# Kernel optimization log

Measured on AMD Instinct MI355X. Metric: run time of the kernel, lower is better.

## Reference

```python
import jax, jax.numpy as jnp
import numpy as np

EPS = 1e-5
GROUPS = 128  # 4 bands * nearest_power_of_2_divisor(256, 32)

def _haar_bands(x):
    # x: (C, H, W), H and W even -> SAME pad is a no-op for 2x2 stride-2 conv.
    # lax conv is cross-correlation: band[i,j] = sum_ab x[2i+a, 2j+b] * k[a,b]
    C, H, W = x.shape
    xr = x.reshape(C, H // 2, 2, W // 2, 2)
    x00 = xr[:, :, 0, :, 0]; x01 = xr[:, :, 0, :, 1]
    x10 = xr[:, :, 1, :, 0]; x11 = xr[:, :, 1, :, 1]
    half = jnp.asarray(0.5, x.dtype)  # (1/sqrt2)^2
    LL = (x00 + x01 + x10 + x11) * half
    HL = (-x00 - x01 + x10 + x11) * half  # outer(h1, h0)
    LH = (-x00 + x01 - x10 + x11) * half  # outer(h0, h1)
    HH = (x00 - x01 - x10 + x11) * half   # outer(h1, h1)
    return LL, HL, LH, HH

def _group_norm(y, scale, bias, groups, eps=EPS):
    C, H, W = y.shape
    yg = y.reshape(groups, C // groups, H, W)
    mean = jnp.mean(yg, axis=(1, 2, 3), keepdims=True)
    var = jnp.mean(jnp.square(yg - mean), axis=(1, 2, 3), keepdims=True)
    yn = ((yg - mean) * jax.lax.rsqrt(var + eps)).reshape(C, H, W)
    return yn * scale[:, None, None] + bias[:, None, None]

def setup_inputs() -> dict:
    key = jax.random.key(0)
    k1, k2 = jax.random.split(key)
    C, H, W, Cout = 256, 256, 256, 512
    x = jax.random.normal(k1, (C, H, W), dtype=jnp.float32)
    gn_scale = jnp.ones((4 * C,), dtype=jnp.float32)
    gn_bias = jnp.zeros((4 * C,), dtype=jnp.float32)
    w_proj = jax.random.normal(k2, (Cout, 4 * C), dtype=jnp.float32) / np.sqrt(4 * C)
    return {"x": x, "gn_scale": gn_scale, "gn_bias": gn_bias, "w_proj": w_proj}

def reference(x, gn_scale, gn_bias, w_proj):
    LL, HL, LH, HH = _haar_bands(x)
    y = jnp.concatenate([LL, HL, LH, HH], axis=0)   # (4C, H/2, W/2)
    y = _group_norm(y, gn_scale, gn_bias, GROUPS)
    y = jnp.einsum('oc,chw->ohw', w_proj, y)        # 1x1 conv, no bias
    y = jax.nn.relu(y)
    # dropout p=0.0 / inference -> identity
    return y
```

## Files before the change

### kernel.cpp

```cpp
#include <hip/hip_runtime.h>
#include <stdint.h>

typedef float  f32x4 __attribute__((ext_vector_type(4)));
typedef short  s16x8 __attribute__((ext_vector_type(8)));
typedef unsigned short u16;

#define GN_EPS 1e-5f


__device__ __forceinline__ u16 f2bf(float f) {
  unsigned u = __float_as_uint(f);
  u += 0x7fffu + ((u >> 16) & 1u);
  return (u16)(u >> 16);
}

__device__ __forceinline__ float wave_red_sum(float v) {
#pragma unroll
  for (int off = 32; off > 0; off >>= 1) v += __shfl_down(v, off, 64);
  return v;
}

__device__ __forceinline__ void gload16(const void* g, void* l) {
  __builtin_amdgcn_global_load_lds(
      (const __attribute__((address_space(1))) uint32_t*)(uintptr_t)g,
      (__attribute__((address_space(3))) uint32_t*)(uintptr_t)l,
      16, 0, 0);
}

__global__ __launch_bounds__(256) void haar_kernel(
    const float* __restrict__ x, u16* __restrict__ yt,
    float* __restrict__ gsum, float* __restrict__ gsqs)
{
  const int t    = threadIdx.x;
  const int cti  = t & 7;
  const int hwi  = t >> 3;
  const int hw0  = blockIdx.x * 64 + hwi * 2;
  const int h    = hw0 >> 7, w = hw0 & 127;
  const int cin0 = blockIdx.y * 64 + cti * 8;

  float sv[4] = {0.f,0.f,0.f,0.f}, qv[4] = {0.f,0.f,0.f,0.f};
  s16x8 ov[2][4];
  f32x4 R0[8], R1[8];

  const float* xb = x + ((size_t)cin0 << 16) + (size_t)(2*h)*256 + (size_t)(2*w);
#pragma unroll
  for (int j = 0; j < 8; ++j) {
    const float* xp = xb + ((size_t)j << 16);
    R0[j] = *(const f32x4*)(xp);
    R1[j] = *(const f32x4*)(xp + 256);
  }
#pragma unroll
  for (int j = 0; j < 8; ++j) {
    f32x4 r0 = R0[j], r1 = R1[j];
#pragma unroll
    for (int p = 0; p < 2; ++p) {
      float x00 = p ? r0.z : r0.x;
      float x01 = p ? r0.w : r0.y;
      float x10 = p ? r1.z : r1.x;
      float x11 = p ? r1.w : r1.y;
      float LL = 0.5f*( x00 + x01 + x10 + x11);
      float HL = 0.5f*(-x00 - x01 + x10 + x11);
      float LH = 0.5f*(-x00 + x01 - x10 + x11);
      float HH = 0.5f*( x00 - x01 - x10 + x11);
      ov[p][0][j] = (short)f2bf(LL);
      ov[p][1][j] = (short)f2bf(HL);
      ov[p][2][j] = (short)f2bf(LH);
      ov[p][3][j] = (short)f2bf(HH);
      sv[0] += LL; qv[0] += LL*LL;
      sv[1] += HL; qv[1] += HL*HL;
      sv[2] += LH; qv[2] += LH*LH;
      sv[3] += HH; qv[3] += HH*HH;
    }
  }

  u16* yb = yt + (size_t)hw0 * 1024 + cin0;
#pragma unroll
  for (int p = 0; p < 2; ++p)
#pragma unroll
    for (int b = 0; b < 4; ++b)
      *(s16x8*)(yb + p*1024 + b*256) = ov[p][b];

#pragma unroll
  for (int k = 0; k < 4; ++k) {
#pragma unroll
    for (int msk = 8; msk < 64; msk <<= 1) {
      sv[k] += __shfl_xor(sv[k], msk, 64);
      qv[k] += __shfl_xor(qv[k], msk, 64);
    }
  }
  __shared__ float red[4][8][8];
  const int lane = t & 63, wv = t >> 6;
  if (lane < 8) {
#pragma unroll
    for (int k = 0; k < 4; ++k) {
      red[wv][lane][k]     = sv[k];
      red[wv][lane][4 + k] = qv[k];
    }
  }
  __syncthreads();
  if (t < 64) {
    int c8 = t & 7, vi = t >> 3;
    float tot = red[0][c8][vi] + red[1][c8][vi] + red[2][c8][vi] + red[3][c8][vi];
    int b = vi & 3;
    int g = b*32 + blockIdx.y*8 + c8;
    if (vi < 4) atomicAdd(&gsum[g], tot);
    else        atomicAdd(&gsqs[g], tot);
  }
}

__global__ __launch_bounds__(256) void wprep_kernel(
    const float* __restrict__ wproj, const float* __restrict__ gsum,
    const float* __restrict__ gsqs, const float* __restrict__ scale,
    const float* __restrict__ bias, u16* __restrict__ wn, float* __restrict__ tvec)
{
  const int o = blockIdx.x;
  const int t = threadIdx.x;
  const float invN = 1.0f / 131072.0f;
  float acc = 0.f;
#pragma unroll
  for (int j = 0; j < 4; ++j) {
    int c = j*256 + t;
    int g = c >> 3;
    float mean = gsum[g] * invN;
    float var  = gsqs[g] * invN - mean * mean;
    float inv  = rsqrtf(var + GN_EPS);
    float a = scale[c] * inv;
    float b = bias[c] - mean * a;
    float wv = wproj[o*1024 + c];
    wn[o*1024 + c] = f2bf(wv * a);
    acc += wv * b;
  }
  acc = wave_red_sum(acc);
  __shared__ float red[4];
  int lane = t & 63, wvi = t >> 6;
  if (lane == 0) red[wvi] = acc;
  __syncthreads();
  if (t == 0) tvec[o] = red[0] + red[1] + red[2] + red[3];
}

#define BM 128
#define BN 128
#define BK 64

__global__ __launch_bounds__(256) void gemm_kernel(
    const u16* __restrict__ A,
    const u16* __restrict__ B,
    const float* __restrict__ tvec,
    float* __restrict__ out)
{
  __shared__ __align__(1024) u16 As[2][BM*BK];
  __shared__ __align__(1024) u16 Bs[2][BN*BK];

  const int tid  = threadIdx.x;
  const int lane = tid & 63, wave = tid >> 6;

  const int bid = blockIdx.x;
  const int cid = (bid & 7) * 64 + (bid >> 3);
  const int m0 = (cid & 3) * BM;
  const int n0 = (cid >> 2) * BN;

  const int wm = wave >> 1, wn_ = wave & 1;
  const int g = lane >> 4, r = lane & 15;

  f32x4 acc[4][4];
#pragma unroll
  for (int i = 0; i < 4; ++i)
#pragma unroll
    for (int j = 0; j < 4; ++j) acc[i][j] = (f32x4)(0.f);

  const int chunk0 = wave * 4;
  int srow[4], soff[4];
#pragma unroll
  for (int ci = 0; ci < 4; ++ci) {
    int linear = (chunk0 + ci) * 1024 + lane * 16;
    srow[ci] = linear >> 7;
    soff[ci] = (linear & 127) ^ ((srow[ci] & 7) << 4);
  }

  auto STAGE = [&](int buf, int k0) {
#pragma unroll
    for (int ci = 0; ci < 4; ++ci) {
      gload16((const char*)(A + (size_t)(m0 + srow[ci])*1024 + k0) + soff[ci],
              (char*)As[buf] + (chunk0 + ci)*1024);
      gload16((const char*)(B + (size_t)(n0 + srow[ci])*1024 + k0) + soff[ci],
              (char*)Bs[buf] + (chunk0 + ci)*1024);
    }
  };

  auto COMPUTE = [&](int buf) {
#pragma unroll
    for (int kk = 0; kk < 2; ++kk) {
      s16x8 av[4], bv[4];
      const int kb = g*16 + kk*64;
#pragma unroll
      for (int m = 0; m < 4; ++m) {
        int row = wm*64 + m*16 + r;
        av[m] = *(const s16x8*)((const char*)As[buf] + row*128 + (kb ^ ((row & 7) << 4)));
      }
#pragma unroll
      for (int n = 0; n < 4; ++n) {
        int row = wn_*64 + n*16 + r;
        bv[n] = *(const s16x8*)((const char*)Bs[buf] + row*128 + (kb ^ ((row & 7) << 4)));
      }
#pragma unroll
      for (int m = 0; m < 4; ++m)
#pragma unroll
        for (int n = 0; n < 4; ++n)
          acc[m][n] = __builtin_amdgcn_mfma_f32_16x16x32_bf16(av[m], bv[n], acc[m][n], 0, 0, 0);
    }
  };

  STAGE(0, 0);
  __syncthreads();
  int cur = 0;
#pragma unroll 1
  for (int t = 0; t < 15; ++t) {
    STAGE(cur ^ 1, (t + 1) * BK);
    COMPUTE(cur);
    __syncthreads();
    cur ^= 1;
  }
  COMPUTE(cur);

#pragma unroll
  for (int m = 0; m < 4; ++m) {
#pragma unroll
    for (int rr = 0; rr < 4; ++rr) {
      int o = m0 + wm*64 + m*16 + g*4 + rr;
      float tv = tvec[o];
      float* op = out + (size_t)o*16384 + n0 + wn_*64 + r;
#pragma unroll
      for (int n = 0; n < 4; ++n) {
        float v = acc[m][n][rr] + tv;
        op[n*16] = v > 0.f ? v : 0.f;
      }
    }
  }
}

extern "C" void kernel_launch(void* const* d_in, const int* in_sizes, int n_in,
                              void* d_out, int out_size, void* d_ws, size_t ws_size,
                              hipStream_t stream)
{
  const float* x  = (const float*)d_in[0];
  const float* sc = (const float*)d_in[1];
  const float* bi = (const float*)d_in[2];
  const float* wp = (const float*)d_in[3];
  float* out = (float*)d_out;

  char* ws = (char*)d_ws;
  float* gsum = (float*)(ws + 0);
  float* gsqs = (float*)(ws + 512);
  float* tv   = (float*)(ws + 9216);
  u16*   wn   = (u16*)(ws + 16384);
  u16*   yt   = (u16*)(ws + 2097152);

  hipMemsetAsync(ws, 0, 1024, stream);
  hipLaunchKernelGGL(haar_kernel,  dim3(256, 4), dim3(256), 0, stream, x, yt, gsum, gsqs);
  hipLaunchKernelGGL(wprep_kernel, dim3(512),    dim3(256), 0, stream, wp, gsum, gsqs, sc, bi, wn, tv);
  hipLaunchKernelGGL(gemm_kernel,  dim3(512),    dim3(256), 0, stream, wn, yt, tv, out);
}
```

Baseline: 139.0 us.

## Restructure GEMM to 256x128 tiles with 8 waves and triple-buffered async loads

The GEMM tile grows to 256 rows with 512 threads (8 waves) and switches from a double-buffered to a triple-buffered LDS pipeline. Global-to-LDS loads for stage t+2 are split into halves and interleaved with the two MFMA sub-steps, using explicit vmcnt waits, raw s_barrier and setprio to keep the matrix units busy. This is meant to hide global load latency and halve B-tile refetch. In exchange it needs more LDS per block (about 144KB), which limits occupancy, and the hand-tuned waitcnt schedule is fragile.

```diff
diff --git a/kernel.cpp b/kernel.cpp
--- a/kernel.cpp
+++ b/kernel.cpp
@@ -138,26 +138,29 @@
   if (t == 0) tvec[o] = red[0] + red[1] + red[2] + red[3];
 }
 
-#define BM 128
+#define BM 256
 #define BN 128
 #define BK 64
-
-__global__ __launch_bounds__(256) void gemm_kernel(
+#define NT 16
+
+#define BAR() asm volatile("s_barrier" ::: "memory")
+
+__global__ __launch_bounds__(512, 2) void gemm_kernel(
     const u16* __restrict__ A,
     const u16* __restrict__ B,
     const float* __restrict__ tvec,
     float* __restrict__ out)
 {
-  __shared__ __align__(1024) u16 As[2][BM*BK];
-  __shared__ __align__(1024) u16 Bs[2][BN*BK];
+  __shared__ __align__(1024) u16 As[3][BM*BK];
+  __shared__ __align__(1024) u16 Bs[3][BN*BK];
 
   const int tid  = threadIdx.x;
   const int lane = tid & 63, wave = tid >> 6;
 
   const int bid = blockIdx.x;
-  const int cid = (bid & 7) * 64 + (bid >> 3);
-  const int m0 = (cid & 3) * BM;
-  const int n0 = (cid >> 2) * BN;
+  const int cid = (bid & 7) * 32 + (bid >> 3);
+  const int m0 = (cid & 1) * BM;
+  const int n0 = (cid >> 1) * BN;
 
   const int wm = wave >> 1, wn_ = wave & 1;
   const int g = lane >> 4, r = lane & 15;
@@ -168,30 +171,50 @@
 #pragma unroll
     for (int j = 0; j < 4; ++j) acc[i][j] = (f32x4)(0.f);
 
-  const int chunk0 = wave * 4;
-  int srow[4], soff[4];
+  int arow[4], aoff[4], brow[2], boff[2];
 #pragma unroll
   for (int ci = 0; ci < 4; ++ci) {
-    int linear = (chunk0 + ci) * 1024 + lane * 16;
-    srow[ci] = linear >> 7;
-    soff[ci] = (linear & 127) ^ ((srow[ci] & 7) << 4);
-  }
-
-  auto STAGE = [&](int buf, int k0) {
-#pragma unroll
-    for (int ci = 0; ci < 4; ++ci) {
-      gload16((const char*)(A + (size_t)(m0 + srow[ci])*1024 + k0) + soff[ci],
-              (char*)As[buf] + (chunk0 + ci)*1024);
-      gload16((const char*)(B + (size_t)(n0 + srow[ci])*1024 + k0) + soff[ci],
-              (char*)Bs[buf] + (chunk0 + ci)*1024);
-    }
+    int lin = ci*8192 + tid*16;
+    arow[ci] = lin >> 7;
+    aoff[ci] = (lin & 127) ^ ((arow[ci] & 7) << 4);
+  }
+#pragma unroll
+  for (int ci = 0; ci < 2; ++ci) {
+    int lin = ci*8192 + tid*16;
+    brow[ci] = lin >> 7;
+    boff[ci] = (lin & 127) ^ ((brow[ci] & 7) << 4);
+  }
+
+  auto LOADA = [&](int buf, int k0, int ci) {
+    gload16((const char*)(A + (size_t)(m0 + arow[ci])*1024 + k0) + aoff[ci],
+            (char*)As[buf] + ci*8192 + tid*16);
   };
-
-  auto COMPUTE = [&](int buf) {
-#pragma unroll
-    for (int kk = 0; kk < 2; ++kk) {
+  auto LOADB = [&](int buf, int k0, int ci) {
+    gload16((const char*)(B + (size_t)(n0 + brow[ci])*1024 + k0) + boff[ci],
+            (char*)Bs[buf] + ci*8192 + tid*16);
+  };
+
+#pragma unroll
+  for (int ci = 0; ci < 4; ++ci) LOADA(0, 0, ci);
+#pragma unroll
+  for (int ci = 0; ci < 2; ++ci) LOADB(0, 0, ci);
+#pragma unroll
+  for (int ci = 0; ci < 4; ++ci) LOADA(1, BK, ci);
+#pragma unroll
+  for (int ci = 0; ci < 2; ++ci) LOADB(1, BK, ci);
+  asm volatile("s_waitcnt vmcnt(6)" ::: "memory");
+  BAR();
+
+#pragma unroll 1
+  for (int t = 0; t < NT; ++t) {
+    const int buf = t % 3;
+    const int nxt = (t + 2) % 3;
+    const int kN  = (t + 2) * BK;
+    const bool pre = (t + 2 < NT);
+
+    {
       s16x8 av[4], bv[4];
-      const int kb = g*16 + kk*64;
+      const int kb = g*16;
 #pragma unroll
       for (int m = 0; m < 4; ++m) {
         int row = wm*64 + m*16 + r;
@@ -202,25 +225,46 @@
         int row = wn_*64 + n*16 + r;
         bv[n] = *(const s16x8*)((const char*)Bs[buf] + row*128 + (kb ^ ((row & 7) << 4)));
       }
+      if (pre) { LOADA(nxt, kN, 0); LOADA(nxt, kN, 1); LOADA(nxt, kN, 2); }
+      BAR();
+      __builtin_amdgcn_s_setprio(1);
 #pragma unroll
       for (int m = 0; m < 4; ++m)
 #pragma unroll
         for (int n = 0; n < 4; ++n)
           acc[m][n] = __builtin_amdgcn_mfma_f32_16x16x32_bf16(av[m], bv[n], acc[m][n], 0, 0, 0);
-    }
-  };
-
-  STAGE(0, 0);
-  __syncthreads();
-  int cur = 0;
-#pragma unroll 1
-  for (int t = 0; t < 15; ++t) {
-    STAGE(cur ^ 1, (t + 1) * BK);
-    COMPUTE(cur);
-    __syncthreads();
-    cur ^= 1;
-  }
-  COMPUTE(cur);
+      __builtin_amdgcn_s_setprio(0);
+      __builtin_amdgcn_sched_barrier(0);
+      BAR();
+    }
+    {
+      s16x8 av[4], bv[4];
+      const int kb = 64 + g*16;
+#pragma unroll
+      for (int m = 0; m < 4; ++m) {
+        int row = wm*64 + m*16 + r;
+        av[m] = *(const s16x8*)((const char*)As[buf] + row*128 + (kb ^ ((row & 7) << 4)));
+      }
+#pragma unroll
+      for (int n = 0; n < 4; ++n) {
+        int row = wn_*64 + n*16 + r;
+        bv[n] = *(const s16x8*)((const char*)Bs[buf] + row*128 + (kb ^ ((row & 7) << 4)));
+      }
+      if (pre) { LOADA(nxt, kN, 3); LOADB(nxt, kN, 0); LOADB(nxt, kN, 1); }
+      BAR();
+      __builtin_amdgcn_s_setprio(1);
+#pragma unroll
+      for (int m = 0; m < 4; ++m)
+#pragma unroll
+        for (int n = 0; n < 4; ++n)
+          acc[m][n] = __builtin_amdgcn_mfma_f32_16x16x32_bf16(av[m], bv[n], acc[m][n], 0, 0, 0);
+      __builtin_amdgcn_s_setprio(0);
+      __builtin_amdgcn_sched_barrier(0);
+      if (t <= NT - 3)      asm volatile("s_waitcnt vmcnt(6)" ::: "memory");
+      else if (t == NT - 2) asm volatile("s_waitcnt vmcnt(0)" ::: "memory");
+      BAR();
+    }
+  }
 
 #pragma unroll
   for (int m = 0; m < 4; ++m) {
@@ -258,5 +302,5 @@
   hipMemsetAsync(ws, 0, 1024, stream);
   hipLaunchKernelGGL(haar_kernel,  dim3(256, 4), dim3(256), 0, stream, x, yt, gsum, gsqs);
   hipLaunchKernelGGL(wprep_kernel, dim3(512),    dim3(256), 0, stream, wp, gsum, gsqs, sc, bi, wn, tv);
-  hipLaunchKernelGGL(gemm_kernel,  dim3(512),    dim3(256), 0, stream, wn, yt, tv, out);
-}
+  hipLaunchKernelGGL(gemm_kernel,  dim3(256),    dim3(512), 0, stream, wn, yt, tv, out);
+}
```

Result: no change. 139.1 us (+0.1%).
